# Kernel optimization log

Measured on AMD Instinct MI355X. Metric: run time of the kernel, lower is better.

The kernel has to match this reference:

```python
import jax, jax.numpy as jnp
import numpy as np

D_MODEL = 64
SEQ_LEN = 9
MAX_SL = 50
TIMESTAMP = 56
ACTION_NUM = 300
BATCH = 65536


def setup_inputs() -> dict:
    key = jax.random.key(0)
    ks = jax.random.split(key, 8)
    input_actions = jax.random.randint(ks[0], (BATCH, SEQ_LEN), 0, ACTION_NUM + 1)
    emb_table = jax.random.normal(ks[1], (ACTION_NUM + 1, D_MODEL), jnp.float32) * 0.02
    emb_table = emb_table.at[0].set(0.0)  # padding_idx=0
    M_w = jax.random.normal(ks[2], (MAX_SL, D_MODEL, D_MODEL), jnp.float32) * 0.05
    M_b = jax.random.normal(ks[3], (MAX_SL, D_MODEL), jnp.float32) * 0.05
    W_w = jax.random.normal(ks[4], (TIMESTAMP, D_MODEL, D_MODEL), jnp.float32) * 0.05
    W_b = jax.random.normal(ks[5], (TIMESTAMP, D_MODEL), jnp.float32) * 0.05
    out_w = jax.random.normal(ks[6], (ACTION_NUM, D_MODEL), jnp.float32) * 0.05
    out_b = jax.random.normal(ks[7], (ACTION_NUM,), jnp.float32) * 0.05
    return {"input_actions": input_actions, "emb_table": emb_table,
            "M_w": M_w, "M_b": M_b, "W_w": W_w, "W_b": W_b,
            "out_w": out_w, "out_b": out_b}


def reference(input_actions, emb_table, M_w, M_b, W_w, W_b, out_w, out_b):
    B, S = input_actions.shape
    d = emb_table.shape[1]
    ae = emb_table[input_actions]              # [B, S, d]
    ae_t = jnp.transpose(ae, (1, 0, 2))        # [S, B, d]
    # per-timestep weight selection, matching M[min(i, len(M)-1)] and W[i % timeStamp]
    m_idx = jnp.minimum(jnp.arange(S), M_w.shape[0] - 1)
    w_idx = jnp.arange(S) % W_w.shape[0]
    Mw, Mb = M_w[m_idx], M_b[m_idx]            # [S, d, d], [S, d]
    Ww, Wb = W_w[w_idx], W_b[w_idx]

    def step(hl, xs):
        x, mw, mb, ww, wb = xs
        # torch Linear: y = x @ W.T + b
        hl = jax.nn.sigmoid(x @ mw.T + mb + hl @ ww.T + wb)
        return hl, None

    hl0 = jnp.zeros((B, d), ae.dtype)
    hl, _ = jax.lax.scan(step, hl0, (ae_t, Mw, Mb, Ww, Wb))
    return hl @ out_w.T + out_b               # [B, actionNum]
```

## Files before the change

### kernel.cpp

```cpp
#include <hip/hip_runtime.h>
#include <hip/hip_bf16.h>


#define SEQ     9
#define DMODEL  64
#define ANUM    300

#define WS_MW   0
#define WS_OW   73728
#define WS_EMB  94208
#define WS_END  113472
#define WS_BSUM_BYTES (WS_END * 2)

#define BSOFF   61440
#define HSOFF   62592
#define SLTOT   78976

typedef __attribute__((ext_vector_type(8))) short  bf16x8;
typedef __attribute__((ext_vector_type(4))) float  f32x4;

#define MFMA __builtin_amdgcn_mfma_f32_16x16x32_bf16

__device__ __forceinline__ unsigned short f2b(float f) {
    union { float f; unsigned int u; } x; x.f = f;
    unsigned int r = x.u + 0x7FFFu + ((x.u >> 16) & 1u);
    return (unsigned short)(r >> 16);
}

__device__ __forceinline__ float sigmoid_fast(float v) {
    return __builtin_amdgcn_rcpf(1.f + __expf(-v));
}

__device__ __forceinline__ void async16(const unsigned short* g, unsigned short* l) {
    __builtin_amdgcn_global_load_lds(
        (const __attribute__((address_space(1))) unsigned int*)g,
        (__attribute__((address_space(3))) unsigned int*)l, 16, 0, 0);
}

#define PP_TOTAL (73728 + 20480 + 19264 + 576)

__global__ void prepack(const float* __restrict__ Mw, const float* __restrict__ Ww,
                        const float* __restrict__ outw, const float* __restrict__ emb,
                        const float* __restrict__ Mb, const float* __restrict__ Wb,
                        unsigned short* __restrict__ wsb, float* __restrict__ bsum)
{
    int t = blockIdx.x * 256 + threadIdx.x;
    if (t < 73728) {
        int s    = t >> 13;
        int r    = t & 8191;
        int kind = r >> 12;
        int f    = r & 4095;
        int nt   = f >> 10;
        int kb   = (f >> 9) & 1;
        int lane = (f >> 3) & 63;
        int j    = f & 7;
        int nr   = nt * 16 + (lane & 15);
        int k    = kb * 32 + ((lane >> 4) << 3) + j;
        const float* src = kind ? Ww : Mw;
        wsb[WS_MW + t] = f2b(src[(s * DMODEL + nr) * DMODEL + k]);
        return;
    }
    t -= 73728;
    if (t < 20480) {
        int j    = t & 7;
        int lane = (t >> 3) & 63;
        int kb   = (t >> 9) & 1;
        int nt   = (t >> 10) & 3;
        int cc   = t >> 12;
        int col  = cc * 64 + nt * 16 + (lane & 15);
        int k    = kb * 32 + ((lane >> 4) << 3) + j;
        float v  = (col < ANUM) ? outw[col * DMODEL + k] : 0.f;
        wsb[WS_OW + t] = f2b(v);
        return;
    }
    t -= 20480;
    if (t < 19264) { wsb[WS_EMB + t] = f2b(emb[t]); return; }
    t -= 19264;
    if (t < 576)   { bsum[t] = Mb[t] + Wb[t]; }
}

__global__ __launch_bounds__(1024, 4)
void carnn_main(const int* __restrict__ acts,
                const unsigned short* __restrict__ wsb,
                const float* __restrict__ bsum,
                const float* __restrict__ outb,
                float* __restrict__ out)
{
    __shared__ __align__(16) unsigned short SL[SLTOT];

    const int tid  = threadIdx.x;
    const int lane = tid & 63;
    const int wv   = tid >> 6;
    const int lrow = lane & 15;
    const int quad = lane >> 4;

    const int brow = (blockIdx.x * 16 + wv) * 16 + lrow;
    const int rowS = brow * SEQ;

    for (int c = wv; c < 120; c += 16) {
        const int goff = (c < 8) ? (c * 512) : ((c + 8) * 512);
        async16(wsb + WS_MW + goff + lane * 8, &SL[c * 512]);
    }
    {
        const unsigned short* bs = (const unsigned short*)bsum;
        if (wv == 13) async16(bs + lane * 8,         &SL[BSOFF]);
        if (wv == 14) async16(bs + 512 + lane * 8,   &SL[BSOFF + 512]);
        if (wv == 15 && lane < 16)
                      async16(bs + 1024 + lane * 8,  &SL[BSOFF + 1024]);
    }

    const unsigned short* Eb = wsb + WS_EMB;
    int idc = acts[rowS];
    bf16x8 xc0 = *(const bf16x8*)(Eb + idc * DMODEL + quad * 8);
    bf16x8 xc1 = *(const bf16x8*)(Eb + idc * DMODEL + 32 + quad * 8);
    int idn = acts[rowS + 1];

    char* const SB = (char*)SL;
    const int swz    = (lrow & 7) << 4;
    const int hbyte  = HSOFF * 2 + wv * 2048 + lrow * 128;
    const int rbyte0 = hbyte + ((quad * 16) ^ swz);
    const int rbyte1 = hbyte + ((64 + quad * 16) ^ swz);

    __syncthreads();

    const float* BSf = (const float*)&SL[BSOFF];

    #pragma unroll
    for (int s = 0; s < SEQ; ++s) {
        bf16x8 xn0, xn1;
        if (s + 1 < SEQ) {
            xn0 = *(const bf16x8*)(Eb + idn * DMODEL + quad * 8);
            xn1 = *(const bf16x8*)(Eb + idn * DMODEL + 32 + quad * 8);
            if (s + 2 < SEQ) idn = acts[rowS + s + 2];
        }
        bf16x8 h0, h1;
        if (s > 0) {
            h0 = *(const bf16x8*)(SB + rbyte0);
            h1 = *(const bf16x8*)(SB + rbyte1);
        }
        const unsigned short* WB;
        if (s == 0)     WB = &SL[0];
        else if (s < 8) WB = &SL[4096 + (s - 1) * 8192];
        else            WB = wsb + WS_MW + 8 * 8192;

        #pragma unroll
        for (int nt = 0; nt < 4; ++nt) {
            const unsigned short* Mf = WB + nt * 1024 + lane * 8;
            bf16x8 am0 = *(const bf16x8*)Mf;
            bf16x8 am1 = *(const bf16x8*)(Mf + 512);
            f32x4 acc = *(const f32x4*)(BSf + s * 64 + nt * 16 + quad * 4);
            acc = MFMA(am0, xc0, acc, 0, 0, 0);
            acc = MFMA(am1, xc1, acc, 0, 0, 0);
            if (s > 0) {
                const unsigned short* Wf = WB + 4096 + nt * 1024 + lane * 8;
                bf16x8 aw0 = *(const bf16x8*)Wf;
                bf16x8 aw1 = *(const bf16x8*)(Wf + 512);
                acc = MFMA(aw0, h0, acc, 0, 0, 0);
                acc = MFMA(aw1, h1, acc, 0, 0, 0);
            }
            unsigned int u0 = (unsigned int)f2b(sigmoid_fast(acc[0]))
                            | ((unsigned int)f2b(sigmoid_fast(acc[1])) << 16);
            unsigned int u1 = (unsigned int)f2b(sigmoid_fast(acc[2]))
                            | ((unsigned int)f2b(sigmoid_fast(acc[3])) << 16);
            *(uint2*)(SB + hbyte + ((nt * 32 + quad * 8) ^ swz)) = make_uint2(u0, u1);
        }
        if (s + 1 < SEQ) { xc0 = xn0; xc1 = xn1; }
    }

    bf16x8 h0 = *(const bf16x8*)(SB + rbyte0);
    bf16x8 h1 = *(const bf16x8*)(SB + rbyte1);
    const unsigned short* OWg = wsb + WS_OW;
    float* orow = out + brow * ANUM;

    #pragma unroll
    for (int t = 0; t < 19; ++t) {
        const int cc = t >> 2, nt = t & 3;
        const unsigned short* Of = OWg + cc * 4096 + nt * 1024 + lane * 8;
        bf16x8 a0 = *(const bf16x8*)Of;
        bf16x8 a1 = *(const bf16x8*)(Of + 512);
        const int col0 = cc * 64 + nt * 16 + quad * 4;

        f32x4 acc;
        if (col0 < ANUM) acc = *(const f32x4*)(outb + col0);
        else             acc = (f32x4){0.f, 0.f, 0.f, 0.f};
        acc = MFMA(a0, h0, acc, 0, 0, 0);
        acc = MFMA(a1, h1, acc, 0, 0, 0);

        if (col0 < ANUM)
            *(f32x4*)(orow + col0) = acc;
    }
}

extern "C" void kernel_launch(void* const* d_in, const int* in_sizes, int n_in,
                              void* d_out, int out_size, void* d_ws, size_t ws_size,
                              hipStream_t stream) {
    const int*   acts = (const int*)  d_in[0];
    const float* emb  = (const float*)d_in[1];
    const float* Mw   = (const float*)d_in[2];
    const float* Mb   = (const float*)d_in[3];
    const float* Ww   = (const float*)d_in[4];
    const float* Wb   = (const float*)d_in[5];
    const float* outw = (const float*)d_in[6];
    const float* outb = (const float*)d_in[7];
    float* out = (float*)d_out;
    (void)in_sizes; (void)n_in; (void)ws_size; (void)out_size;

    unsigned short* wsb = (unsigned short*)d_ws;
    float* bsum = (float*)((char*)d_ws + WS_BSUM_BYTES);

    prepack<<<(PP_TOTAL + 255) / 256, 256, 0, stream>>>(Mw, Ww, outw, emb, Mb, Wb, wsb, bsum);
    carnn_main<<<65536 / 256, 1024, 0, stream>>>(acts, wsb, bsum, outb, out);
}
```

Measured before the change: 120.4 us.

## Prefetch step-8 weights into registers and stage output weights in LDS

Step 8's M and W fragments were read from global memory inside the recurrence. They are now loaded into registers during step 7, so the latency overlaps with step 7's compute. After the recurrence, the output projection weights and output bias are copied asynchronously into the reused LDS region between two block barriers, so the 19-tile projection reads from LDS instead of global or cache. Output stores become nontemporal to avoid polluting cache. The change adds register pressure (16 extra vector registers), which matters under launch bounds of 1024 threads with 4 blocks, and it adds two extra block-wide syncs.

```diff
diff --git a/kernel.cpp b/kernel.cpp
--- a/kernel.cpp
+++ b/kernel.cpp
@@ -124,6 +124,7 @@
     __syncthreads();
 
     const float* BSf = (const float*)&SL[BSOFF];
+    bf16x8 s8m[8], s8w[8];
 
     #pragma unroll
     for (int s = 0; s < SEQ; ++s) {
@@ -133,28 +134,45 @@
             xn1 = *(const bf16x8*)(Eb + idn * DMODEL + 32 + quad * 8);
             if (s + 2 < SEQ) idn = acts[rowS + s + 2];
         }
+        if (s == 7) {
+            const unsigned short* G8 = wsb + WS_MW + 8 * 8192;
+            #pragma unroll
+            for (int q2 = 0; q2 < 4; ++q2) {
+                s8m[q2 * 2]     = *(const bf16x8*)(G8 + q2 * 1024 + lane * 8);
+                s8m[q2 * 2 + 1] = *(const bf16x8*)(G8 + q2 * 1024 + 512 + lane * 8);
+            }
+        }
         bf16x8 h0, h1;
         if (s > 0) {
             h0 = *(const bf16x8*)(SB + rbyte0);
             h1 = *(const bf16x8*)(SB + rbyte1);
         }
-        const unsigned short* WB;
-        if (s == 0)     WB = &SL[0];
-        else if (s < 8) WB = &SL[4096 + (s - 1) * 8192];
-        else            WB = wsb + WS_MW + 8 * 8192;
+        const unsigned short* WB = (s == 0) ? &SL[0] : &SL[4096 + (s - 1) * 8192];
 
         #pragma unroll
         for (int nt = 0; nt < 4; ++nt) {
-            const unsigned short* Mf = WB + nt * 1024 + lane * 8;
-            bf16x8 am0 = *(const bf16x8*)Mf;
-            bf16x8 am1 = *(const bf16x8*)(Mf + 512);
+            bf16x8 am0, am1;
+            if (s < 8) {
+                const unsigned short* Mf = WB + nt * 1024 + lane * 8;
+                am0 = *(const bf16x8*)Mf;
+                am1 = *(const bf16x8*)(Mf + 512);
+            } else {
+                am0 = s8m[nt * 2];
+                am1 = s8m[nt * 2 + 1];
+            }
             f32x4 acc = *(const f32x4*)(BSf + s * 64 + nt * 16 + quad * 4);
             acc = MFMA(am0, xc0, acc, 0, 0, 0);
             acc = MFMA(am1, xc1, acc, 0, 0, 0);
             if (s > 0) {
-                const unsigned short* Wf = WB + 4096 + nt * 1024 + lane * 8;
-                bf16x8 aw0 = *(const bf16x8*)Wf;
-                bf16x8 aw1 = *(const bf16x8*)(Wf + 512);
+                bf16x8 aw0, aw1;
+                if (s < 8) {
+                    const unsigned short* Wf = WB + 4096 + nt * 1024 + lane * 8;
+                    aw0 = *(const bf16x8*)Wf;
+                    aw1 = *(const bf16x8*)(Wf + 512);
+                } else {
+                    aw0 = s8w[nt * 2];
+                    aw1 = s8w[nt * 2 + 1];
+                }
                 acc = MFMA(aw0, h0, acc, 0, 0, 0);
                 acc = MFMA(aw1, h1, acc, 0, 0, 0);
             }
@@ -164,30 +182,49 @@
                             | ((unsigned int)f2b(sigmoid_fast(acc[3])) << 16);
             *(uint2*)(SB + hbyte + ((nt * 32 + quad * 8) ^ swz)) = make_uint2(u0, u1);
         }
+        if (s == 7) {
+            const unsigned short* G8 = wsb + WS_MW + 8 * 8192 + 4096;
+            #pragma unroll
+            for (int q2 = 0; q2 < 4; ++q2) {
+                s8w[q2 * 2]     = *(const bf16x8*)(G8 + q2 * 1024 + lane * 8);
+                s8w[q2 * 2 + 1] = *(const bf16x8*)(G8 + q2 * 1024 + 512 + lane * 8);
+            }
+        }
         if (s + 1 < SEQ) { xc0 = xn0; xc1 = xn1; }
     }
 
     bf16x8 h0 = *(const bf16x8*)(SB + rbyte0);
     bf16x8 h1 = *(const bf16x8*)(SB + rbyte1);
-    const unsigned short* OWg = wsb + WS_OW;
+
+    __syncthreads();
+    for (int c = wv; c < 40; c += 16)
+        async16(wsb + WS_OW + c * 512 + lane * 8, &SL[c * 512]);
+    {
+        const unsigned short* ob = (const unsigned short*)outb;
+        if (wv == 12)               async16(ob + lane * 8,       &SL[BSOFF]);
+        if (wv == 13 && lane < 11)  async16(ob + 512 + lane * 8, &SL[BSOFF + 512]);
+    }
+    __syncthreads();
+
+    const float* OBf = (const float*)&SL[BSOFF];
     float* orow = out + brow * ANUM;
 
     #pragma unroll
     for (int t = 0; t < 19; ++t) {
         const int cc = t >> 2, nt = t & 3;
-        const unsigned short* Of = OWg + cc * 4096 + nt * 1024 + lane * 8;
+        const unsigned short* Of = &SL[cc * 4096 + nt * 1024 + lane * 8];
         bf16x8 a0 = *(const bf16x8*)Of;
         bf16x8 a1 = *(const bf16x8*)(Of + 512);
         const int col0 = cc * 64 + nt * 16 + quad * 4;
 
         f32x4 acc;
-        if (col0 < ANUM) acc = *(const f32x4*)(outb + col0);
+        if (col0 < ANUM) acc = *(const f32x4*)(OBf + col0);
         else             acc = (f32x4){0.f, 0.f, 0.f, 0.f};
         acc = MFMA(a0, h0, acc, 0, 0, 0);
         acc = MFMA(a1, h1, acc, 0, 0, 0);
 
         if (col0 < ANUM)
-            *(f32x4*)(orow + col0) = acc;
+            __builtin_nontemporal_store(acc, (f32x4*)(orow + col0));
     }
 }
 
```

Result: slower. 159.7 us (+32.5%).
